# Kernel tuning notes

Hardware: AMD Instinct MI355X
Metric: run time of the kernel (lower is better)

Reference implementation:

```python
import jax, jax.numpy as jnp
import numpy as np

K_NEIGHBORS = 5  # sklearn KNNImputer default n_neighbors, weights='uniform'


def _impute_feature(Xz, present):
    # Xz: [N, T1] feature values with 0 at missing entries; present: [N, T1] bool.
    # sklearn nan_euclidean distance: sqrt(T1/cnt * sum_valid (x_i - y_i)^2),
    # valid dims = both present; cnt==0 -> excluded (treated as inf here).
    T1 = Xz.shape[1]
    pf = present.astype(Xz.dtype)
    sq = Xz * Xz
    d2 = sq @ pf.T + pf @ sq.T - 2.0 * (Xz @ Xz.T)  # [N, N]
    cnt = pf @ pf.T
    d2 = jnp.maximum(d2, 0.0) * (jnp.asarray(T1, Xz.dtype) / jnp.maximum(cnt, 1.0))
    dist = jnp.sqrt(d2)
    dist = jnp.where(cnt > 0, dist, jnp.inf)
    # distances only pick neighbors (piecewise-constant wrt values)
    dist = jax.lax.stop_gradient(dist)

    def impute_col(xcol, prescol):
        # donors must have a value in this column and a finite distance
        d = jnp.where(prescol[None, :], dist, jnp.inf)  # [N, N]
        negv, idx = jax.lax.top_k(-d, K_NEIGHBORS)       # k smallest distances
        sel_ok = jnp.isfinite(negv)                      # [N, K]
        vals = xcol[idx]                                 # [N, K] donor values
        cntk = sel_ok.sum(-1)
        mean_k = (vals * sel_ok).sum(-1) / jnp.maximum(cntk, 1)
        # fallback: observed column mean when no valid donor (sklearn behavior)
        colmean = (xcol * prescol).sum() / jnp.maximum(prescol.sum(), 1)
        imput = jnp.where(cntk > 0, mean_k, colmean)
        return jnp.where(prescol, xcol, imput)  # [N]

    # vmap over the T1 columns -> [T1, N]
    return jax.vmap(impute_col, in_axes=(1, 1))(Xz, present)


def reference(x_all, mask):
    # x_all: [T1, N, D_in] stacked node features (steps + output graph)
    # mask:  [T1, N] int, 1 = missing (original code: last channel of x)
    T1, N, D_in = x_all.shape
    C = D_in - 1  # output_node_dim
    present = (mask == 0).T  # [N, T1]
    outs = []
    for c in range(C):
        X = x_all[..., c].T                      # [N, T1]
        Xz = jnp.where(present, X, 0.0)
        steps = _impute_feature(Xz, present)     # [T1, N]
        outs.append(steps[-1])                   # last step = output graph
    return jnp.stack(outs, axis=-1)              # [N, C] -> h_v


def setup_inputs() -> dict:
    key = jax.random.key(0)
    k1, k2 = jax.random.split(key)
    x_all = jax.random.normal(k1, (17, 2048, 9), dtype=jnp.float32)
    mask = jax.random.randint(k2, (17, 2048), 0, 2, dtype=jnp.int32)
    return {"x_all": x_all, "mask": mask}
```

## Files before the change

kernel.cpp:

```cpp
#include <hip/hip_runtime.h>
#include <math.h>

#define T1 17
#define NN 2048
#define DIN 9
#define CC 8
#define KK 5
#define NSTR 5
#define NDCAP (NSTR * 256)
#define NQCAP 1280
#define LPAD (NDCAP + 8)
#define NU (NDCAP / 64)

#define XD_BYTES (T1 * NN * CC * 4)

__global__ __launch_bounds__(1024) void prep_kernel(
    const float* __restrict__ x_all, const int* __restrict__ mask,
    unsigned* __restrict__ pm, int* __restrict__ dlist,
    unsigned* __restrict__ pmd, int* __restrict__ qlist,
    float* __restrict__ colmean, int* __restrict__ cnts,
    float* __restrict__ out) {
  __shared__ unsigned long long dbal[32];
  __shared__ int dpre[33], qpre[33];
  __shared__ float wsum[16][CC];
  const int tid = threadIdx.x;
  const int lane = tid & 63, w = tid >> 6;

  unsigned m0 = 0, m1 = 0;
#pragma unroll
  for (int t = 0; t < T1; ++t) {
    m0 |= (mask[t * NN + tid] == 0 ? 1u : 0u) << t;
    m1 |= (mask[t * NN + tid + 1024] == 0 ? 1u : 0u) << t;
  }
  pm[tid] = m0;
  pm[tid + 1024] = m1;
  const bool v0 = (m0 >> 16) & 1u, v1 = (m1 >> 16) & 1u;
  const unsigned long long b0 = __ballot(v0), b1 = __ballot(v1);
  if (lane == 0) { dbal[w] = b0; dbal[16 + w] = b1; }

  float s[CC];
#pragma unroll
  for (int c = 0; c < CC; ++c) s[c] = 0.f;
  if (v0) {
    const float* row = x_all + ((size_t)16 * NN + tid) * DIN;
#pragma unroll
    for (int c = 0; c < CC; ++c) { const float v = row[c]; s[c] = v; out[tid * CC + c] = v; }
  }
  if (v1) {
    const float* row = x_all + ((size_t)16 * NN + tid + 1024) * DIN;
#pragma unroll
    for (int c = 0; c < CC; ++c) { const float v = row[c]; s[c] += v; out[(tid + 1024) * CC + c] = v; }
  }
#pragma unroll
  for (int off = 32; off > 0; off >>= 1) {
#pragma unroll
    for (int c = 0; c < CC; ++c) s[c] += __shfl_down(s[c], off);
  }
  if (lane == 0) {
#pragma unroll
    for (int c = 0; c < CC; ++c) wsum[w][c] = s[c];
  }
  __syncthreads();

  if (tid == 0) {
    int a = 0, b = 0;
    for (int g = 0; g < 32; ++g) {
      dpre[g] = a;
      qpre[g] = b;
      const int p = (int)__popcll(dbal[g]);
      a += p;
      b += 64 - p;
    }
    dpre[32] = a;
    qpre[32] = b;
    cnts[0] = a;
    cnts[1] = b;
  }
  __syncthreads();

  const unsigned long long ltm = (1ull << lane) - 1ull;
  if (v0) {
    const int p = dpre[w] + (int)__popcll(b0 & ltm);
    dlist[p] = tid; pmd[p] = m0;
  } else {
    const int p = qpre[w] + (int)__popcll((~b0) & ltm);
    qlist[p] = tid;
  }
  if (v1) {
    const int p = dpre[16 + w] + (int)__popcll(b1 & ltm);
    dlist[p] = tid + 1024; pmd[p] = m1;
  } else {
    const int p = qpre[16 + w] + (int)__popcll((~b1) & ltm);
    qlist[p] = tid + 1024;
  }

  if (tid < CC) {
    float tot = 0.f;
#pragma unroll
    for (int ww = 0; ww < 16; ++ww) tot += wsum[ww][tid];
    colmean[tid] = tot / fmaxf((float)dpre[32], 1.f);
  }
}

__global__ void transpose_kernel(const float* __restrict__ x_all,
                                 const int* __restrict__ dlist,
                                 const int* __restrict__ cnts,
                                 float* __restrict__ xd) {
  const int u = blockIdx.x * 256 + threadIdx.x;
  if (u >= T1 * NN * CC) return;
  const int t = u / (NN * CC);
  const int rem = u % (NN * CC);
  const int dn = rem >> 3;
  const int c = rem & 7;
  if (dn < cnts[0]) xd[u] = x_all[((size_t)t * NN + dlist[dn]) * DIN + c];
}

__global__ __launch_bounds__(512, 3) void knn_main(
    const float* __restrict__ x_all, const float* __restrict__ xd,
    const unsigned* __restrict__ pm, const unsigned* __restrict__ pmd,
    const int* __restrict__ qlist, const int* __restrict__ cnts,
    const float* __restrict__ colmean, float* __restrict__ out) {
  __shared__ float sdist[CC][LPAD];
  __shared__ float qlds[16][CC];
  __shared__ float rcp17[32];
  const int nq = cnts[1];
  const int bid = blockIdx.x;
  if (bid >= nq) return;
  const int i = qlist[bid];
  const int ndon = cnts[0];
  const unsigned mi = pm[i];
  const int tid = threadIdx.x;

  if (tid < 32) rcp17[tid] = 17.f / (float)tid;
  if (tid < 16 * CC)
    qlds[tid >> 3][tid & 7] = x_all[((size_t)(tid >> 3) * NN + i) * DIN + (tid & 7)];
  __syncthreads();

  const int qd = tid & 1;
  const int c0 = qd * 4;
  const int dg = tid >> 1;
  const int lane = tid & 63;
  const int w = tid >> 6;

  for (int s = 0; s < NSTR; ++s) {
    const int dn = dg + 256 * s;
    float a0 = 0.f, a1 = 0.f, a2 = 0.f, a3 = 0.f;
    unsigned msk = 0u;
    if (256 * s < ndon) {
      msk = (dn < ndon) ? (mi & pmd[dn]) : 0u;
      const float* dbase = xd + (size_t)dn * CC + c0;
      for (unsigned tm = mi & 0xFFFFu; tm; tm &= tm - 1u) {
        const int t = __ffs(tm) - 1;
        const float4 qv = *(const float4*)&qlds[t][c0];
        const float4 dv = *(const float4*)(dbase + (size_t)t * (NN * CC));
        const float fl = (float)((msk >> t) & 1u);
        float e;
        e = qv.x - dv.x; a0 = fmaf(e * e, fl, a0);
        e = qv.y - dv.y; a1 = fmaf(e * e, fl, a1);
        e = qv.z - dv.z; a2 = fmaf(e * e, fl, a2);
        e = qv.w - dv.w; a3 = fmaf(e * e, fl, a3);
      }
    }
    const int cnt = __popc(msk);
    const float sc = rcp17[cnt & 31];
    const bool ok = cnt > 0;
    sdist[c0 + 0][dn] = ok ? sqrtf(a0 * sc) : INFINITY;
    sdist[c0 + 1][dn] = ok ? sqrtf(a1 * sc) : INFINITY;
    sdist[c0 + 2][dn] = ok ? sqrtf(a2 * sc) : INFINITY;
    sdist[c0 + 3][dn] = ok ? sqrtf(a3 * sc) : INFINITY;
  }
  __syncthreads();

  float dvr[NU];
#pragma unroll
  for (int u = 0; u < NU; ++u) dvr[u] = sdist[w][u * 64 + lane];

  float sum = 0.f;
  int cn = 0;
#pragma unroll
  for (int k = 0; k < KK; ++k) {
    float g = dvr[0];
#pragma unroll
    for (int u = 1; u < NU; ++u) g = fminf(g, dvr[u]);
#pragma unroll
    for (int off = 32; off > 0; off >>= 1) g = fminf(g, __shfl_xor(g, off));
    if (g < INFINITY) {
      int jloc = 0x7FFFFFFF;
#pragma unroll
      for (int u = NU - 1; u >= 0; --u)
        if (dvr[u] == g) jloc = u * 64 + lane;
      int jg = jloc;
#pragma unroll
      for (int off = 32; off > 0; off >>= 1) jg = min(jg, __shfl_xor(jg, off));
      const int jgs = __builtin_amdgcn_readfirstlane(jg);
      const int tu = jgs >> 6, tl = jgs & 63;
#pragma unroll
      for (int u = 0; u < NU; ++u)
        if (u == tu) dvr[u] = (lane == tl) ? INFINITY : dvr[u];
      sum += xd[((size_t)16 * NN + jgs) * CC + w];
      ++cn;
    }
  }
  if (lane == 0) out[i * CC + w] = (cn > 0) ? sum / (float)cn : colmean[w];
}

extern "C" void kernel_launch(void* const* d_in, const int* in_sizes, int n_in,
                              void* d_out, int out_size, void* d_ws, size_t ws_size,
                              hipStream_t stream) {
  const float* x_all = (const float*)d_in[0];
  const int* mask = (const int*)d_in[1];
  float* out = (float*)d_out;

  char* ws = (char*)d_ws;
  float* xd = (float*)ws;
  unsigned* pm = (unsigned*)(ws + XD_BYTES);
  int* dlist = (int*)(ws + XD_BYTES + NN * 4);
  unsigned* pmd = (unsigned*)(ws + XD_BYTES + NN * 8);
  int* qlist = (int*)(ws + XD_BYTES + NN * 12);
  float* colmean = (float*)(ws + XD_BYTES + NN * 16);
  int* cnts = (int*)(ws + XD_BYTES + NN * 16 + CC * 4);

  prep_kernel<<<1, 1024, 0, stream>>>(x_all, mask, pm, dlist, pmd, qlist, colmean, cnts, out);
  transpose_kernel<<<(T1 * NN * CC + 255) / 256, 256, 0, stream>>>(x_all, dlist, cnts, xd);
  knn_main<<<NQCAP, 512, 0, stream>>>(x_all, xd, pm, pmd, qlist, cnts, colmean, out);
}
```

Measured before the change: 47.21 us.

## Interchange stripe and timestep loops, process two timesteps per iteration

The distance accumulation loop is restructured so the outer loop walks the query's present timesteps, two at a time, and the inner unrolled loop covers all donor stripes with per-stripe register accumulators. The aim is to issue more independent global loads per iteration and reuse each query LDS read across stripes. A zero padding row (t=16) in qlds handles odd timestep counts, since its mask bit is zero. This raises register pressure (20 accumulators plus masks), which under launch_bounds(512,3) may cause spills.

```diff
diff --git a/kernel.cpp b/kernel.cpp
--- a/kernel.cpp
+++ b/kernel.cpp
@@ -121,7 +121,7 @@
     const int* __restrict__ qlist, const int* __restrict__ cnts,
     const float* __restrict__ colmean, float* __restrict__ out) {
   __shared__ float sdist[CC][LPAD];
-  __shared__ float qlds[16][CC];
+  __shared__ float qlds[T1][CC];
   __shared__ float rcp17[32];
   const int nq = cnts[1];
   const int bid = blockIdx.x;
@@ -134,6 +134,7 @@
   if (tid < 32) rcp17[tid] = 17.f / (float)tid;
   if (tid < 16 * CC)
     qlds[tid >> 3][tid & 7] = x_all[((size_t)(tid >> 3) * NN + i) * DIN + (tid & 7)];
+  if (tid >= 16 * CC && tid < 17 * CC) qlds[16][tid & 7] = 0.f;
   __syncthreads();
 
   const int qd = tid & 1;
@@ -142,32 +143,55 @@
   const int lane = tid & 63;
   const int w = tid >> 6;
 
+  float a0[NSTR], a1[NSTR], a2[NSTR], a3[NSTR];
+  unsigned ms[NSTR];
+#pragma unroll
   for (int s = 0; s < NSTR; ++s) {
     const int dn = dg + 256 * s;
-    float a0 = 0.f, a1 = 0.f, a2 = 0.f, a3 = 0.f;
-    unsigned msk = 0u;
-    if (256 * s < ndon) {
-      msk = (dn < ndon) ? (mi & pmd[dn]) : 0u;
-      const float* dbase = xd + (size_t)dn * CC + c0;
-      for (unsigned tm = mi & 0xFFFFu; tm; tm &= tm - 1u) {
-        const int t = __ffs(tm) - 1;
-        const float4 qv = *(const float4*)&qlds[t][c0];
-        const float4 dv = *(const float4*)(dbase + (size_t)t * (NN * CC));
-        const float fl = (float)((msk >> t) & 1u);
+    ms[s] = (dn < ndon) ? (mi & pmd[dn]) : 0u;
+    a0[s] = a1[s] = a2[s] = a3[s] = 0.f;
+  }
+  const int nstr_act = (ndon + 255) >> 8;
+
+  unsigned tm = mi & 0xFFFFu;
+  while (tm) {
+    const int t0 = __ffs(tm) - 1;
+    tm &= tm - 1u;
+    const int t1 = tm ? (__ffs(tm) - 1) : 16;
+    tm = tm ? (tm & (tm - 1u)) : 0u;
+    const float4 qv0 = *(const float4*)&qlds[t0][c0];
+    const float4 qv1 = *(const float4*)&qlds[t1][c0];
+#pragma unroll
+    for (int s = 0; s < NSTR; ++s) {
+      if (s < nstr_act) {
+        const int dn = dg + 256 * s;
+        const float4 dv0 = *(const float4*)&xd[((size_t)t0 * NN + dn) * CC + c0];
+        const float4 dv1 = *(const float4*)&xd[((size_t)t1 * NN + dn) * CC + c0];
+        const float fl0 = (float)((ms[s] >> t0) & 1u);
+        const float fl1 = (float)((ms[s] >> t1) & 1u);
         float e;
-        e = qv.x - dv.x; a0 = fmaf(e * e, fl, a0);
-        e = qv.y - dv.y; a1 = fmaf(e * e, fl, a1);
-        e = qv.z - dv.z; a2 = fmaf(e * e, fl, a2);
-        e = qv.w - dv.w; a3 = fmaf(e * e, fl, a3);
+        e = qv0.x - dv0.x; a0[s] = fmaf(e * e, fl0, a0[s]);
+        e = qv0.y - dv0.y; a1[s] = fmaf(e * e, fl0, a1[s]);
+        e = qv0.z - dv0.z; a2[s] = fmaf(e * e, fl0, a2[s]);
+        e = qv0.w - dv0.w; a3[s] = fmaf(e * e, fl0, a3[s]);
+        e = qv1.x - dv1.x; a0[s] = fmaf(e * e, fl1, a0[s]);
+        e = qv1.y - dv1.y; a1[s] = fmaf(e * e, fl1, a1[s]);
+        e = qv1.z - dv1.z; a2[s] = fmaf(e * e, fl1, a2[s]);
+        e = qv1.w - dv1.w; a3[s] = fmaf(e * e, fl1, a3[s]);
       }
     }
-    const int cnt = __popc(msk);
+  }
+
+#pragma unroll
+  for (int s = 0; s < NSTR; ++s) {
+    const int dn = dg + 256 * s;
+    const int cnt = __popc(ms[s]);
     const float sc = rcp17[cnt & 31];
     const bool ok = cnt > 0;
-    sdist[c0 + 0][dn] = ok ? sqrtf(a0 * sc) : INFINITY;
-    sdist[c0 + 1][dn] = ok ? sqrtf(a1 * sc) : INFINITY;
-    sdist[c0 + 2][dn] = ok ? sqrtf(a2 * sc) : INFINITY;
-    sdist[c0 + 3][dn] = ok ? sqrtf(a3 * sc) : INFINITY;
+    sdist[c0 + 0][dn] = ok ? sqrtf(a0[s] * sc) : INFINITY;
+    sdist[c0 + 1][dn] = ok ? sqrtf(a1[s] * sc) : INFINITY;
+    sdist[c0 + 2][dn] = ok ? sqrtf(a2[s] * sc) : INFINITY;
+    sdist[c0 + 3][dn] = ok ? sqrtf(a3[s] * sc) : INFINITY;
   }
   __syncthreads();
 
```

Measured after the change: 45.38 us. 1.04x faster.
